# Kernel optimization log

Measured on AMD Instinct MI355X. Metric: run time of the kernel, lower is better.

Reference implementation:

```python
import jax, jax.numpy as jnp
import numpy as np

NUM_CARDS = 2
NUM_ACTIONS = 3
BATCH = 4194304


def setup_inputs() -> dict:
    key = jax.random.key(0)
    k1, k2, k3 = jax.random.split(key, 3)
    cards_0 = jax.random.randint(k1, (BATCH,), 0, NUM_CARDS, dtype=jnp.int32)
    W = jax.random.normal(k2, (NUM_ACTIONS, NUM_CARDS), dtype=jnp.float32) * 0.5
    b = jax.random.normal(k3, (NUM_ACTIONS,), dtype=jnp.float32) * 0.1
    return {"cards_0": cards_0, "W": W, "b": b}


def reference(cards_0, W, b):
    B = cards_0.shape[0]
    # one_hot(i % C) @ W.T + b collapses to W[:, c] + b for each card c.
    # logp: (C, A) counterfactual log-policy per card.
    logp = jax.nn.log_softmax(W.T + b[None, :], axis=-1)
    # Independent multinomial(1) sample per (batch, card) pair -> (B, C) action ids.
    skey = jax.random.key(42)
    cf_action = jax.random.categorical(skey, logp, axis=-1, shape=(B, NUM_CARDS))
    # log prob of the sampled one-hot under Multinomial(1) == log p of chosen action.
    card_idx = jnp.arange(NUM_CARDS)[None, :]            # (1, C)
    log_cf = logp[card_idx, cf_action]                   # (B, C)
    # Action actually taken for the dealt card.
    u0 = jnp.take_along_axis(cf_action, cards_0[:, None].astype(jnp.int32), axis=1)[:, 0]
    # Beliefs: normalized indicator of which cards would have produced u0.
    weights = (u0[:, None] == cf_action).astype(jnp.float32)  # (B, C)
    beliefs = weights / jnp.sum(weights, axis=-1, keepdims=True)
    return (u0, beliefs, log_cf)
```

## Files before the change

kernel.cpp:

```cpp
#include <hip/hip_runtime.h>

#pragma clang fp contract(off)

#define TPB 256

__device__ __forceinline__ uint32_t rotl32(uint32_t x, uint32_t n) {
  return (x << n) | (x >> (32u - n));
}

__device__ __forceinline__ uint32_t threefry_draw32(uint32_t j) {
  const uint32_t ks1 = 42u;
  const uint32_t ks2 = 0x1BD11BDAu ^ 42u;
  uint32_t x0 = 0u;
  uint32_t x1 = j + ks1;

#define TFR(r) { x0 += x1; x1 = rotl32(x1, r); x1 ^= x0; }
  TFR(13u) TFR(15u) TFR(26u) TFR(6u)   x0 += ks1; x1 += ks2 + 1u;
  TFR(17u) TFR(29u) TFR(16u) TFR(24u)  x0 += ks2; x1 += 0u  + 2u;
  TFR(13u) TFR(15u) TFR(26u) TFR(6u)   x0 += 0u;  x1 += ks1 + 3u;
  TFR(17u) TFR(29u) TFR(16u) TFR(24u)  x0 += ks1; x1 += ks2 + 4u;
  TFR(13u) TFR(15u) TFR(26u) TFR(6u)   x0 += ks2; x1 += 0u  + 5u;
#undef TFR
  return x0 ^ x1;
}

__device__ __forceinline__ float xla_logf(float xin) {
  uint32_t bits = __float_as_uint(xin);
  int emm0 = (int)(bits >> 23) - 0x7f;
  float m = __uint_as_float((bits & 0x007fffffu) | 0x3f000000u);
  float e = (float)emm0 + 1.0f;

  bool mask = m < 0.707106781186547524f;
  float tmp = mask ? m : 0.0f;
  m = m - 1.0f;
  e = e - (mask ? 1.0f : 0.0f);
  m = m + tmp;

  float x2 = m * m;
  float x3 = x2 * m;

  float y  =  7.0376836292e-2f * m + -1.1514610310e-1f;
  float y1 = -1.2420140846e-1f * m +  1.4249322787e-1f;
  float y2 =  2.0000714765e-1f * m + -2.4999993993e-1f;
  y  = y  * m +  1.1676998740e-1f;
  y1 = y1 * m + -1.6668057665e-1f;
  y2 = y2 * m +  3.3333331174e-1f;
  y  = y * x3 + y1;
  y  = y * x3 + y2;
  y  = y * x3;

  float t1 = -2.12194440e-4f * e;
  float t2 = 0.5f * x2;
  y = y + t1;
  m = m - t2;
  float t3 = 0.693359375f * e;
  m = m + y;
  m = m + t3;
  return m;
}

__device__ __forceinline__ float xla_expf(float xin) {
  float xc = fminf(xin, 88.3762626647950f);
  xc = fmaxf(xc, -88.3762626647949f);

  float fx = floorf(xc * 1.44269504088896341f + 0.5f);
  float tmp = 0.693359375f * fx;
  float z   = -2.12194440e-4f * fx;
  float x = xc - tmp;
  x = x - z;
  z = x * x;

  float y = x * 1.9875691500e-4f + 1.3981999507e-3f;
  y = y * x + 8.3334519073e-3f;
  y = y * x + 4.1665795894e-2f;
  y = y * x + 1.6666665459e-1f;
  y = y * x + 5.0000001201e-1f;
  y = y * z + x;
  y = y + 1.0f;

  int n = (int)fx;
  float p2n = __uint_as_float((uint32_t)(n + 0x7f) << 23);
  return fmaxf(y * p2n, xin);
}

__device__ __forceinline__ float ref_gumbel(uint32_t bits) {
  float f = __uint_as_float((bits >> 9) | 0x3f800000u) - 1.0f;
  float u = (f == 0.0f) ? 1.17549435082228750797e-38f : f;
  float l1 = xla_logf(u);
  float l2 = xla_logf(-l1);
  return -l2;
}

__global__ void __launch_bounds__(TPB) sample_kernel(
    const int* __restrict__ cards, const float* __restrict__ W,
    const float* __restrict__ bvec,
    float* __restrict__ out_u0, float* __restrict__ out_beliefs,
    float* __restrict__ out_logcf, int B) {
  __shared__ float lp_s[6];
  if (threadIdx.x == 0) {
    for (int c = 0; c < 2; ++c) {
      float x0 = W[0 * 2 + c] + bvec[0];
      float x1 = W[1 * 2 + c] + bvec[1];
      float x2 = W[2 * 2 + c] + bvec[2];
      float mx = fmaxf(fmaxf(fmaxf(-__builtin_inff(), x0), x1), x2);
      float s0 = x0 - mx, s1 = x1 - mx, s2 = x2 - mx;
      float e0 = xla_expf(s0);
      float e1 = xla_expf(s1);
      float e2 = xla_expf(s2);
      float se = (e0 + e1) + e2;
      float lse = xla_logf(se);
      lp_s[c * 3 + 0] = s0 - lse;
      lp_s[c * 3 + 1] = s1 - lse;
      lp_s[c * 3 + 2] = s2 - lse;
    }
  }
  __syncthreads();

  int b = blockIdx.x * TPB + threadIdx.x;
  if (b >= B) return;

  float lp[6];
#pragma unroll
  for (int i = 0; i < 6; ++i) lp[i] = lp_s[i];

  uint32_t base = (uint32_t)b * 6u;

  int cf[2];
  float lcf[2];
#pragma unroll
  for (int c = 0; c < 2; ++c) {
    float s0 = ref_gumbel(threefry_draw32(base + (uint32_t)(c * 3) + 0u)) + lp[c * 3 + 0];
    float s1 = ref_gumbel(threefry_draw32(base + (uint32_t)(c * 3) + 1u)) + lp[c * 3 + 1];
    float s2 = ref_gumbel(threefry_draw32(base + (uint32_t)(c * 3) + 2u)) + lp[c * 3 + 2];
    int best_a = 0;
    float best = s0;
    if (s1 > best) { best = s1; best_a = 1; }
    if (s2 > best) { best = s2; best_a = 2; }
    cf[c] = best_a;
    lcf[c] = lp[c * 3 + best_a];
  }

  int card = cards[b];
  int u0 = (card == 0) ? cf[0] : cf[1];
  float w0 = (u0 == cf[0]) ? 1.0f : 0.0f;
  float w1 = (u0 == cf[1]) ? 1.0f : 0.0f;
  float half_or_one = ((w0 + w1) > 1.5f) ? 0.5f : 1.0f;

  out_u0[b] = (float)u0;
  reinterpret_cast<float2*>(out_beliefs)[b] = make_float2(w0 * half_or_one, w1 * half_or_one);
  reinterpret_cast<float2*>(out_logcf)[b]  = make_float2(lcf[0], lcf[1]);
}

extern "C" void kernel_launch(void* const* d_in, const int* in_sizes, int n_in,
                              void* d_out, int out_size, void* d_ws, size_t ws_size,
                              hipStream_t stream) {
  (void)n_in; (void)out_size; (void)d_ws; (void)ws_size;
  const int* cards = (const int*)d_in[0];
  const float* W   = (const float*)d_in[1];
  const float* bv  = (const float*)d_in[2];
  float* out = (float*)d_out;

  int B = in_sizes[0];
  sample_kernel<<<(B + TPB - 1) / TPB, TPB, 0, stream>>>(
      cards, W, bv, out, out + (size_t)B, out + (size_t)3 * B, B);
}
```

Before: 172.6 us.

## Pack Gumbel log math into float2 vectors and precompute log-policy in separate kernel

Rewrites the double-log Gumbel transform to work on two-element float vectors so the compiler can emit packed FP32 instructions (v_pk_fma/v_pk_mul on CDNA), halving the ALU instruction count of the dominant math. The per-block log-softmax computation and __syncthreads are moved into a tiny setup kernel that writes logp to workspace, which the main kernel then reads from global memory. This removes block-level serialization but adds a second launch and a dependency on the workspace.

```diff
diff --git a/kernel.cpp b/kernel.cpp
--- a/kernel.cpp
+++ b/kernel.cpp
@@ -3,6 +3,8 @@
 #pragma clang fp contract(off)
 
 #define TPB 256
+
+typedef float f32x2 __attribute__((ext_vector_type(2)));
 
 __device__ __forceinline__ uint32_t rotl32(uint32_t x, uint32_t n) {
   return (x << n) | (x >> (32u - n));
@@ -29,16 +31,13 @@
   int emm0 = (int)(bits >> 23) - 0x7f;
   float m = __uint_as_float((bits & 0x007fffffu) | 0x3f000000u);
   float e = (float)emm0 + 1.0f;
-
   bool mask = m < 0.707106781186547524f;
   float tmp = mask ? m : 0.0f;
   m = m - 1.0f;
   e = e - (mask ? 1.0f : 0.0f);
   m = m + tmp;
-
   float x2 = m * m;
   float x3 = x2 * m;
-
   float y  =  7.0376836292e-2f * m + -1.1514610310e-1f;
   float y1 = -1.2420140846e-1f * m +  1.4249322787e-1f;
   float y2 =  2.0000714765e-1f * m + -2.4999993993e-1f;
@@ -48,7 +47,6 @@
   y  = y * x3 + y1;
   y  = y * x3 + y2;
   y  = y * x3;
-
   float t1 = -2.12194440e-4f * e;
   float t2 = 0.5f * x2;
   y = y + t1;
@@ -62,14 +60,12 @@
 __device__ __forceinline__ float xla_expf(float xin) {
   float xc = fminf(xin, 88.3762626647950f);
   xc = fmaxf(xc, -88.3762626647949f);
-
   float fx = floorf(xc * 1.44269504088896341f + 0.5f);
   float tmp = 0.693359375f * fx;
   float z   = -2.12194440e-4f * fx;
   float x = xc - tmp;
   x = x - z;
   z = x * x;
-
   float y = x * 1.9875691500e-4f + 1.3981999507e-3f;
   y = y * x + 8.3334519073e-3f;
   y = y * x + 4.1665795894e-2f;
@@ -77,27 +73,67 @@
   y = y * x + 5.0000001201e-1f;
   y = y * z + x;
   y = y + 1.0f;
-
   int n = (int)fx;
   float p2n = __uint_as_float((uint32_t)(n + 0x7f) << 23);
   return fmaxf(y * p2n, xin);
 }
 
-__device__ __forceinline__ float ref_gumbel(uint32_t bits) {
-  float f = __uint_as_float((bits >> 9) | 0x3f800000u) - 1.0f;
-  float u = (f == 0.0f) ? 1.17549435082228750797e-38f : f;
-  float l1 = xla_logf(u);
-  float l2 = xla_logf(-l1);
-  return -l2;
-}
-
-__global__ void __launch_bounds__(TPB) sample_kernel(
-    const int* __restrict__ cards, const float* __restrict__ W,
-    const float* __restrict__ bvec,
-    float* __restrict__ out_u0, float* __restrict__ out_beliefs,
-    float* __restrict__ out_logcf, int B) {
-  __shared__ float lp_s[6];
-  if (threadIdx.x == 0) {
+__device__ __forceinline__ f32x2 xla_logf_pk(f32x2 xin) {
+  uint32_t b0 = __float_as_uint(xin.x);
+  uint32_t b1 = __float_as_uint(xin.y);
+  f32x2 m;
+  m.x = __uint_as_float((b0 & 0x007fffffu) | 0x3f000000u);
+  m.y = __uint_as_float((b1 & 0x007fffffu) | 0x3f000000u);
+  bool mk0 = m.x < 0.707106781186547524f;
+  bool mk1 = m.y < 0.707106781186547524f;
+  f32x2 e;
+  e.x = (float)((int)(b0 >> 23) - 126 - (mk0 ? 1 : 0));
+  e.y = (float)((int)(b1 >> 23) - 126 - (mk1 ? 1 : 0));
+  f32x2 tmp;
+  tmp.x = mk0 ? m.x : 0.0f;
+  tmp.y = mk1 ? m.y : 0.0f;
+  m = m - 1.0f;
+  m = m + tmp;
+
+  f32x2 x2 = m * m;
+  f32x2 x3 = x2 * m;
+
+  f32x2 y  = m * 7.0376836292e-2f  + -1.1514610310e-1f;
+  f32x2 y1 = m * -1.2420140846e-1f +  1.4249322787e-1f;
+  f32x2 y2 = m * 2.0000714765e-1f  + -2.4999993993e-1f;
+  y  = y  * m +  1.1676998740e-1f;
+  y1 = y1 * m + -1.6668057665e-1f;
+  y2 = y2 * m +  3.3333331174e-1f;
+  y  = y * x3 + y1;
+  y  = y * x3 + y2;
+  y  = y * x3;
+
+  f32x2 t1 = e * -2.12194440e-4f;
+  f32x2 t2 = x2 * 0.5f;
+  y = y + t1;
+  m = m - t2;
+  f32x2 t3 = e * 0.693359375f;
+  m = m + y;
+  m = m + t3;
+  return m;
+}
+
+__device__ __forceinline__ f32x2 log_neg_log_u(uint32_t r0, uint32_t r1) {
+  f32x2 f;
+  f.x = __uint_as_float((r0 >> 9) | 0x3f800000u);
+  f.y = __uint_as_float((r1 >> 9) | 0x3f800000u);
+  f = f - 1.0f;
+  f32x2 u;
+  u.x = (f.x == 0.0f) ? 1.17549435082228750797e-38f : f.x;
+  u.y = (f.y == 0.0f) ? 1.17549435082228750797e-38f : f.y;
+  f32x2 l1 = xla_logf_pk(u);
+  return xla_logf_pk(-l1);
+}
+
+__global__ void setup_logp(const float* __restrict__ W,
+                           const float* __restrict__ bvec,
+                           float* __restrict__ logp) {
+  if (threadIdx.x == 0 && blockIdx.x == 0) {
     for (int c = 0; c < 2; ++c) {
       float x0 = W[0 * 2 + c] + bvec[0];
       float x1 = W[1 * 2 + c] + bvec[1];
@@ -109,58 +145,73 @@
       float e2 = xla_expf(s2);
       float se = (e0 + e1) + e2;
       float lse = xla_logf(se);
-      lp_s[c * 3 + 0] = s0 - lse;
-      lp_s[c * 3 + 1] = s1 - lse;
-      lp_s[c * 3 + 2] = s2 - lse;
+      logp[c * 3 + 0] = s0 - lse;
+      logp[c * 3 + 1] = s1 - lse;
+      logp[c * 3 + 2] = s2 - lse;
     }
   }
-  __syncthreads();
-
+}
+
+__global__ void __launch_bounds__(TPB) sample_kernel(
+    const int* __restrict__ cards, const float* __restrict__ lp_g,
+    float* __restrict__ out_u0, float* __restrict__ out_beliefs,
+    float* __restrict__ out_logcf, int B) {
   int b = blockIdx.x * TPB + threadIdx.x;
   if (b >= B) return;
 
   float lp[6];
 #pragma unroll
-  for (int i = 0; i < 6; ++i) lp[i] = lp_s[i];
+  for (int i = 0; i < 6; ++i) lp[i] = lp_g[i];
 
   uint32_t base = (uint32_t)b * 6u;
 
-  int cf[2];
-  float lcf[2];
+  uint32_t r[6];
 #pragma unroll
-  for (int c = 0; c < 2; ++c) {
-    float s0 = ref_gumbel(threefry_draw32(base + (uint32_t)(c * 3) + 0u)) + lp[c * 3 + 0];
-    float s1 = ref_gumbel(threefry_draw32(base + (uint32_t)(c * 3) + 1u)) + lp[c * 3 + 1];
-    float s2 = ref_gumbel(threefry_draw32(base + (uint32_t)(c * 3) + 2u)) + lp[c * 3 + 2];
-    int best_a = 0;
-    float best = s0;
-    if (s1 > best) { best = s1; best_a = 1; }
-    if (s2 > best) { best = s2; best_a = 2; }
-    cf[c] = best_a;
-    lcf[c] = lp[c * 3 + best_a];
+  for (int k = 0; k < 6; ++k) r[k] = threefry_draw32(base + (uint32_t)k);
+
+  f32x2 s[3];
+#pragma unroll
+  for (int k = 0; k < 3; ++k) {
+    f32x2 l2 = log_neg_log_u(r[k], r[k + 3]);
+    f32x2 lpk;
+    lpk.x = lp[k];
+    lpk.y = lp[3 + k];
+    s[k] = lpk - l2;
   }
 
+  int a0 = 0; float best0 = s[0].x;
+  if (s[1].x > best0) { best0 = s[1].x; a0 = 1; }
+  if (s[2].x > best0) { best0 = s[2].x; a0 = 2; }
+  int a1 = 0; float best1 = s[0].y;
+  if (s[1].y > best1) { best1 = s[1].y; a1 = 1; }
+  if (s[2].y > best1) { best1 = s[2].y; a1 = 2; }
+
+  float lcf0 = lp[a0];
+  float lcf1 = lp[3 + a1];
+
   int card = cards[b];
-  int u0 = (card == 0) ? cf[0] : cf[1];
-  float w0 = (u0 == cf[0]) ? 1.0f : 0.0f;
-  float w1 = (u0 == cf[1]) ? 1.0f : 0.0f;
+  int u0 = (card == 0) ? a0 : a1;
+  float w0 = (u0 == a0) ? 1.0f : 0.0f;
+  float w1 = (u0 == a1) ? 1.0f : 0.0f;
   float half_or_one = ((w0 + w1) > 1.5f) ? 0.5f : 1.0f;
 
   out_u0[b] = (float)u0;
   reinterpret_cast<float2*>(out_beliefs)[b] = make_float2(w0 * half_or_one, w1 * half_or_one);
-  reinterpret_cast<float2*>(out_logcf)[b]  = make_float2(lcf[0], lcf[1]);
+  reinterpret_cast<float2*>(out_logcf)[b]  = make_float2(lcf0, lcf1);
 }
 
 extern "C" void kernel_launch(void* const* d_in, const int* in_sizes, int n_in,
                               void* d_out, int out_size, void* d_ws, size_t ws_size,
                               hipStream_t stream) {
-  (void)n_in; (void)out_size; (void)d_ws; (void)ws_size;
+  (void)n_in; (void)out_size; (void)ws_size;
   const int* cards = (const int*)d_in[0];
   const float* W   = (const float*)d_in[1];
   const float* bv  = (const float*)d_in[2];
   float* out = (float*)d_out;
+  float* lp  = (float*)d_ws;
 
   int B = in_sizes[0];
+  setup_logp<<<1, 64, 0, stream>>>(W, bv, lp);
   sample_kernel<<<(B + TPB - 1) / TPB, TPB, 0, stream>>>(
-      cards, W, bv, out, out + (size_t)B, out + (size_t)3 * B, B);
-}
+      cards, lp, out, out + (size_t)B, out + (size_t)3 * B, B);
+}
```

After: 168.3 us. 1.03x faster.
